# Kernel optimization log

Measured on AMD Instinct MI355X. Metric: run time of the kernel, lower is better.

Reference implementation:

```python
import jax, jax.numpy as jnp
import numpy as np

N = 100000        # nodes
E = 1600000       # edges (avg degree 16)
D_IN = 128        # input_dim
HID = 128         # hidden
L = 2             # num_layers
EPS = 1e-5        # LayerNorm eps (torch default)


def setup_inputs() -> dict:
    key = jax.random.key(0)
    ks = jax.random.split(key, 5)
    x = jax.random.normal(ks[0], (N, D_IN), dtype=jnp.float32)
    edge_index = jax.random.randint(ks[1], (2, E), 0, N, dtype=jnp.int64)
    e_feat = jax.random.uniform(ks[2], (E,), dtype=jnp.float32)
    # nn.Linear(input_dim, hidden): weight [hidden, input_dim], bias [hidden]
    lin_w = jax.random.normal(ks[3], (HID, D_IN), dtype=jnp.float32) / np.float32(np.sqrt(D_IN))
    lin_b = jax.random.normal(ks[4], (HID,), dtype=jnp.float32) * 0.01
    ln_scale = jnp.ones((L, HID), dtype=jnp.float32)
    ln_bias = jnp.zeros((L, HID), dtype=jnp.float32)
    return {"x": x, "edge_index": edge_index, "e_feat": e_feat,
            "lin_w": lin_w, "lin_b": lin_b,
            "ln_scale": ln_scale, "ln_bias": ln_bias}


def _layernorm(h, scale, bias):
    mu = jnp.mean(h, axis=-1, keepdims=True)
    var = jnp.mean(jnp.square(h - mu), axis=-1, keepdims=True)
    return (h - mu) * jax.lax.rsqrt(var + EPS) * scale + bias


def reference(x, edge_index, e_feat, lin_w, lin_b, ln_scale, ln_bias):
    src, dst = edge_index[0], edge_index[1]
    h = x @ lin_w.T + lin_b            # [N, HID]
    ori = h
    for i in range(L):
        if i != 0:                      # res=True
            h = h + ori
        h = _layernorm(h, ln_scale[i], ln_bias[i])   # norm=True
        h = jax.nn.relu(h)              # relu=True; dp=0 -> dropout no-op
        # GraphConv(weight=False, bias=False): weighted SpMM aggregation
        msg = h[src] * e_feat[:, None]  # [E, HID]
        h = jax.ops.segment_sum(msg, dst, num_segments=N)  # [N, HID]
    return h
```

## Files before the change

kernel.cpp:

```cpp
#include <hip/hip_runtime.h>


constexpr int N_NODES = 100000;
constexpr int N_EDGES = 1600000;
constexpr int HID     = 128;
constexpr int CAP     = 48;
constexpr float LN_EPS = 1e-5f;

typedef __attribute__((ext_vector_type(8))) short short8;
typedef __attribute__((ext_vector_type(4))) float floatx4;

__device__ inline unsigned pack_bf16x2(float a, float b) {
    unsigned ua = __float_as_uint(a), ub = __float_as_uint(b);
    ua += 0x7fff + ((ua >> 16) & 1);
    ub += 0x7fff + ((ub >> 16) & 1);
    return (ua >> 16) | (ub & 0xffff0000u);
}

__global__ void k_prepw(const float* __restrict__ W, unsigned* __restrict__ Wb) {
    int i = blockIdx.x * 256 + threadIdx.x;
    float2 w = ((const float2*)W)[i];
    Wb[i] = pack_bf16x2(w.x, w.y);
}

__global__ void k_scatter(const int* __restrict__ ei, const float* __restrict__ ef,
                          int* __restrict__ cnt, int2* __restrict__ cwp) {
    int e = blockIdx.x * 256 + threadIdx.x;
    if (e >= N_EDGES) return;
    int s = ei[e];
    int d = ei[N_EDGES + e];
    int pos = atomicAdd(&cnt[d], 1);
    if (pos < CAP) cwp[(size_t)d * CAP + pos] = make_int2(s, __float_as_int(ef[e]));
}

__global__ __launch_bounds__(256) void k_gemm_mfma(const float* __restrict__ x,
                                                   const unsigned* __restrict__ Wb,
                                                   const float* __restrict__ bias,
                                                   const float* __restrict__ lns,
                                                   const float* __restrict__ lnb,
                                                   float* __restrict__ h0,
                                                   unsigned* __restrict__ hact) {
    __shared__ __align__(16) char smem[128 * 136 * 2 + 64 * 136 * 2];
    ushort (*Ws)[136] = (ushort(*)[136])smem;
    ushort (*Xs)[136] = (ushort(*)[136])(smem + 128 * 136 * 2);
    float  (*Hs)[132] = (float(*)[132])smem;

    const int t    = threadIdx.x;
    const int row0 = blockIdx.x * 64;

    {
        const uint4* Wg = (const uint4*)Wb;
#pragma unroll
        for (int i = 0; i < 8; ++i) {
            int g = t + 256 * i;
            int r = g >> 4;
            int c = (g & 15) * 8;
            uint4 v = Wg[g];
            *(uint4*)&Ws[r][c] = v;
        }
    }
    {
        const float4* xg = (const float4*)x;
        const int base = blockIdx.x * 2048;
#pragma unroll
        for (int i = 0; i < 8; ++i) {
            int f = t + 256 * i;
            int g = base + f;
            float4 v = make_float4(0.f, 0.f, 0.f, 0.f);
            if (g < N_NODES * 32) v = xg[g];
            int r = f >> 5;
            int c = (f & 31) * 4;
            uint2 p = make_uint2(pack_bf16x2(v.x, v.y), pack_bf16x2(v.z, v.w));
            *(uint2*)&Xs[r][c] = p;
        }
    }
    __syncthreads();

    const int wv   = t >> 6;
    const int l    = t & 63;
    const int mrow = l & 15;
    const int kq   = l >> 4;

    floatx4 acc[8];
#pragma unroll
    for (int i = 0; i < 8; ++i) acc[i] = (floatx4){0.f, 0.f, 0.f, 0.f};

#pragma unroll
    for (int ks = 0; ks < 4; ++ks) {
        short8 a = *(const short8*)&Xs[wv * 16 + mrow][ks * 32 + kq * 8];
#pragma unroll
        for (int tc = 0; tc < 8; ++tc) {
            short8 b = *(const short8*)&Ws[tc * 16 + mrow][ks * 32 + kq * 8];
            acc[tc] = __builtin_amdgcn_mfma_f32_16x16x32_bf16(a, b, acc[tc], 0, 0, 0);
        }
    }
    __syncthreads();

#pragma unroll
    for (int tc = 0; tc < 8; ++tc)
#pragma unroll
        for (int r = 0; r < 4; ++r)
            Hs[wv * 16 + kq * 4 + r][tc * 16 + mrow] = acc[tc][r];
    __syncthreads();

    const float2 b2  = ((const float2*)bias)[l];
    const float2 sc2 = ((const float2*)lns)[l];
    const float2 bb2 = ((const float2*)lnb)[l];
    for (int rr = 0; rr < 16; ++rr) {
        const int lrow = wv * 16 + rr;
        const int grow = row0 + lrow;
        if (grow >= N_NODES) break;
        float2 v = *(const float2*)&Hs[lrow][l * 2];
        v.x += b2.x; v.y += b2.y;
        ((float2*)h0)[(size_t)grow * 64 + l] = v;
        float s  = v.x + v.y;
        float s2 = v.x * v.x + v.y * v.y;
#pragma unroll
        for (int m = 1; m < 64; m <<= 1) {
            s  += __shfl_xor(s, m);
            s2 += __shfl_xor(s2, m);
        }
        const float mu   = s * (1.0f / 128.0f);
        const float var  = s2 * (1.0f / 128.0f) - mu * mu;
        const float rstd = rsqrtf(var + LN_EPS);
        float y0 = fmaxf((v.x - mu) * rstd * sc2.x + bb2.x, 0.0f);
        float y1 = fmaxf((v.y - mu) * rstd * sc2.y + bb2.y, 0.0f);
        hact[(size_t)grow * 64 + l] = pack_bf16x2(y0, y1);
    }
}

__global__ __launch_bounds__(256) void k_spmm_ln(const int* __restrict__ cnt,
                                                 const int2* __restrict__ cwp,
                                                 const unsigned* __restrict__ Hb,
                                                 const float* __restrict__ ori,
                                                 const float* __restrict__ lns,
                                                 const float* __restrict__ lnb,
                                                 unsigned* __restrict__ hout) {
    const int wid  = (blockIdx.x * 256 + threadIdx.x) >> 6;
    const int lane = threadIdx.x & 63;

    const int deg = __builtin_amdgcn_readfirstlane(min(cnt[wid], CAP));
    const int beg = wid * CAP;
    const int end = beg + deg;

    float2 acc = make_float2(0.0f, 0.0f);
    int e = beg;
    for (; e + 4 <= end; e += 4) {
        int2 c0 = cwp[e], c1 = cwp[e + 1], c2 = cwp[e + 2], c3 = cwp[e + 3];
        unsigned v0 = Hb[(size_t)c0.x * 64 + lane];
        unsigned v1 = Hb[(size_t)c1.x * 64 + lane];
        unsigned v2 = Hb[(size_t)c2.x * 64 + lane];
        unsigned v3 = Hb[(size_t)c3.x * 64 + lane];
        float w0 = __int_as_float(c0.y), w1 = __int_as_float(c1.y);
        float w2 = __int_as_float(c2.y), w3 = __int_as_float(c3.y);
        acc.x += w0 * __uint_as_float(v0 << 16) + w1 * __uint_as_float(v1 << 16)
               + w2 * __uint_as_float(v2 << 16) + w3 * __uint_as_float(v3 << 16);
        acc.y += w0 * __uint_as_float(v0 & 0xffff0000u) + w1 * __uint_as_float(v1 & 0xffff0000u)
               + w2 * __uint_as_float(v2 & 0xffff0000u) + w3 * __uint_as_float(v3 & 0xffff0000u);
    }
    for (; e < end; ++e) {
        int2 c0 = cwp[e];
        unsigned v0 = Hb[(size_t)c0.x * 64 + lane];
        float w0 = __int_as_float(c0.y);
        acc.x += w0 * __uint_as_float(v0 << 16);
        acc.y += w0 * __uint_as_float(v0 & 0xffff0000u);
    }

    float2 o = ((const float2*)ori)[(size_t)wid * 64 + lane];
    float vx = acc.x + o.x, vy = acc.y + o.y;
    float s  = vx + vy;
    float s2 = vx * vx + vy * vy;
#pragma unroll
    for (int m = 1; m < 64; m <<= 1) {
        s  += __shfl_xor(s, m);
        s2 += __shfl_xor(s2, m);
    }
    const float mu   = s * (1.0f / 128.0f);
    const float var  = s2 * (1.0f / 128.0f) - mu * mu;
    const float rstd = rsqrtf(var + LN_EPS);
    const int c = lane * 2;
    float y0 = fmaxf((vx - mu) * rstd * lns[c]     + lnb[c],     0.0f);
    float y1 = fmaxf((vy - mu) * rstd * lns[c + 1] + lnb[c + 1], 0.0f);
    hout[(size_t)wid * 64 + lane] = pack_bf16x2(y0, y1);
}

__global__ __launch_bounds__(256) void k_spmm_out(const int* __restrict__ cnt,
                                                  const int2* __restrict__ cwp,
                                                  const unsigned* __restrict__ Hb,
                                                  float* __restrict__ out) {
    const int wid  = (blockIdx.x * 256 + threadIdx.x) >> 6;
    const int lane = threadIdx.x & 63;

    const int deg = __builtin_amdgcn_readfirstlane(min(cnt[wid], CAP));
    const int beg = wid * CAP;
    const int end = beg + deg;

    float2 acc = make_float2(0.0f, 0.0f);
    int e = beg;
    for (; e + 4 <= end; e += 4) {
        int2 c0 = cwp[e], c1 = cwp[e + 1], c2 = cwp[e + 2], c3 = cwp[e + 3];
        unsigned v0 = Hb[(size_t)c0.x * 64 + lane];
        unsigned v1 = Hb[(size_t)c1.x * 64 + lane];
        unsigned v2 = Hb[(size_t)c2.x * 64 + lane];
        unsigned v3 = Hb[(size_t)c3.x * 64 + lane];
        float w0 = __int_as_float(c0.y), w1 = __int_as_float(c1.y);
        float w2 = __int_as_float(c2.y), w3 = __int_as_float(c3.y);
        acc.x += w0 * __uint_as_float(v0 << 16) + w1 * __uint_as_float(v1 << 16)
               + w2 * __uint_as_float(v2 << 16) + w3 * __uint_as_float(v3 << 16);
        acc.y += w0 * __uint_as_float(v0 & 0xffff0000u) + w1 * __uint_as_float(v1 & 0xffff0000u)
               + w2 * __uint_as_float(v2 & 0xffff0000u) + w3 * __uint_as_float(v3 & 0xffff0000u);
    }
    for (; e < end; ++e) {
        int2 c0 = cwp[e];
        unsigned v0 = Hb[(size_t)c0.x * 64 + lane];
        float w0 = __int_as_float(c0.y);
        acc.x += w0 * __uint_as_float(v0 << 16);
        acc.y += w0 * __uint_as_float(v0 & 0xffff0000u);
    }
    ((float2*)out)[(size_t)wid * 64 + lane] = acc;
}

extern "C" void kernel_launch(void* const* d_in, const int* in_sizes, int n_in,
                              void* d_out, int out_size, void* d_ws, size_t ws_size,
                              hipStream_t stream) {
    const float* x   = (const float*)d_in[0];
    const int*   ei  = (const int*)d_in[1];
    const float* ef  = (const float*)d_in[2];
    const float* W   = (const float*)d_in[3];
    const float* b   = (const float*)d_in[4];
    const float* lns = (const float*)d_in[5];
    const float* lnb = (const float*)d_in[6];
    float* out = (float*)d_out;

    float* h0 = out;

    unsigned* hact  = (unsigned*)d_ws;
    unsigned* hact2 = hact + (size_t)N_NODES * 64;
    int*      cnt   = (int*)(hact2 + (size_t)N_NODES * 64);
    unsigned* Wb    = (unsigned*)(cnt + N_NODES);
    int2*     cwp   = (int2*)(Wb + 8192);

    const int eb = (N_EDGES + 255) / 256;
    const int wb = N_NODES * 64 / 256;

    hipMemsetAsync(cnt, 0, N_NODES * sizeof(int), stream);
    k_prepw<<<32, 256, 0, stream>>>(W, Wb);
    k_scatter<<<eb, 256, 0, stream>>>(ei, ef, cnt, cwp);

    k_gemm_mfma<<<(N_NODES + 63) / 64, 256, 0, stream>>>(x, Wb, b, lns, lnb, h0, hact);

    k_spmm_ln<<<wb, 256, 0, stream>>>(cnt, cwp, hact, h0, lns + HID, lnb + HID, hact2);
    k_spmm_out<<<wb, 256, 0, stream>>>(cnt, cwp, hact2, out);
}
```

Baseline: 388.2 us.

## Build compact CSR via two-level bucket sort instead of padded atomic scatter

```diff
diff --git a/kernel.cpp b/kernel.cpp
--- a/kernel.cpp
+++ b/kernel.cpp
@@ -4,7 +4,8 @@
 constexpr int N_NODES = 100000;
 constexpr int N_EDGES = 1600000;
 constexpr int HID     = 128;
-constexpr int CAP     = 48;
+constexpr int NBKT    = (N_NODES + 511) / 512;
+constexpr int BCAP    = 9216;
 constexpr float LN_EPS = 1e-5f;
 
 typedef __attribute__((ext_vector_type(8))) short short8;
@@ -23,14 +24,147 @@
     Wb[i] = pack_bf16x2(w.x, w.y);
 }
 
-__global__ void k_scatter(const int* __restrict__ ei, const float* __restrict__ ef,
-                          int* __restrict__ cnt, int2* __restrict__ cwp) {
-    int e = blockIdx.x * 256 + threadIdx.x;
-    if (e >= N_EDGES) return;
-    int s = ei[e];
-    int d = ei[N_EDGES + e];
-    int pos = atomicAdd(&cnt[d], 1);
-    if (pos < CAP) cwp[(size_t)d * CAP + pos] = make_int2(s, __float_as_int(ef[e]));
+__global__ __launch_bounds__(256) void k_bin(const int* __restrict__ ei,
+                                             const float* __restrict__ ef,
+                                             int* __restrict__ gcur,
+                                             int* __restrict__ gbufDst,
+                                             int2* __restrict__ gbufSW) {
+    __shared__ int cnt[NBKT];
+    __shared__ int incl[256];
+    __shared__ int gbase[NBKT];
+    __shared__ int sdst[2048];
+    __shared__ int2 ssw[2048];
+    const int t = threadIdx.x;
+
+    for (int e0 = blockIdx.x * 2048; e0 < N_EDGES; e0 += gridDim.x * 2048) {
+        for (int i = t; i < NBKT; i += 256) cnt[i] = 0;
+        __syncthreads();
+
+        const int nE = min(2048, N_EDGES - e0);
+        int ed[8], es[8], ep[8]; float ew[8];
+        const int base = e0 + t * 8;
+        if (base + 8 <= N_EDGES) {
+            int4 s0 = *(const int4*)&ei[base];
+            int4 s1 = *(const int4*)&ei[base + 4];
+            int4 d0 = *(const int4*)&ei[N_EDGES + base];
+            int4 d1 = *(const int4*)&ei[N_EDGES + base + 4];
+            float4 w0 = *(const float4*)&ef[base];
+            float4 w1 = *(const float4*)&ef[base + 4];
+            es[0]=s0.x; es[1]=s0.y; es[2]=s0.z; es[3]=s0.w;
+            es[4]=s1.x; es[5]=s1.y; es[6]=s1.z; es[7]=s1.w;
+            ed[0]=d0.x; ed[1]=d0.y; ed[2]=d0.z; ed[3]=d0.w;
+            ed[4]=d1.x; ed[5]=d1.y; ed[6]=d1.z; ed[7]=d1.w;
+            ew[0]=w0.x; ew[1]=w0.y; ew[2]=w0.z; ew[3]=w0.w;
+            ew[4]=w1.x; ew[5]=w1.y; ew[6]=w1.z; ew[7]=w1.w;
+#pragma unroll
+            for (int k = 0; k < 8; ++k) ep[k] = atomicAdd(&cnt[ed[k] >> 9], 1);
+        } else {
+#pragma unroll
+            for (int k = 0; k < 8; ++k) {
+                int idx = base + k;
+                if (idx < N_EDGES) {
+                    es[k] = ei[idx]; ed[k] = ei[N_EDGES + idx]; ew[k] = ef[idx];
+                    ep[k] = atomicAdd(&cnt[ed[k] >> 9], 1);
+                } else ed[k] = -1;
+            }
+        }
+        __syncthreads();
+
+        int v = (t < NBKT) ? cnt[t] : 0;
+        incl[t] = v;
+        for (int o = 1; o < 256; o <<= 1) {
+            __syncthreads();
+            int u = (t >= o) ? incl[t - o] : 0;
+            __syncthreads();
+            incl[t] += u;
+        }
+        __syncthreads();
+        if (t < NBKT) gbase[t] = atomicAdd(&gcur[t], v);
+        __syncthreads();
+
+#pragma unroll
+        for (int k = 0; k < 8; ++k) {
+            if (ed[k] < 0) continue;
+            int b = ed[k] >> 9;
+            int idx = incl[b] - cnt[b] + ep[k];
+            sdst[idx] = ed[k];
+            ssw[idx] = make_int2(es[k], __float_as_int(ew[k]));
+        }
+        __syncthreads();
+
+        for (int j = t; j < nE; j += 256) {
+            int d = sdst[j];
+            int b = d >> 9;
+            int pos = gbase[b] + (j - (incl[b] - cnt[b]));
+            if (pos < BCAP) {
+                gbufDst[(size_t)b * BCAP + pos] = d;
+                gbufSW [(size_t)b * BCAP + pos] = ssw[j];
+            }
+        }
+        __syncthreads();
+    }
+}
+
+__global__ __launch_bounds__(256) void k_scan(const int* __restrict__ gcur,
+                                              int* __restrict__ cbase,
+                                              int* __restrict__ rp) {
+    __shared__ int s[256];
+    const int t = threadIdx.x;
+    int v = (t < NBKT) ? min(gcur[t], BCAP) : 0;
+    s[t] = v;
+    for (int o = 1; o < 256; o <<= 1) {
+        __syncthreads();
+        int u = (t >= o) ? s[t - o] : 0;
+        __syncthreads();
+        s[t] += u;
+    }
+    __syncthreads();
+    if (t < NBKT) cbase[t] = s[t] - v;
+    if (t == NBKT - 1) rp[N_NODES] = s[t];
+}
+
+__global__ __launch_bounds__(512) void k_build(const int* __restrict__ gcur,
+                                               const int* __restrict__ cbase,
+                                               const int* __restrict__ gbufDst,
+                                               const int2* __restrict__ gbufSW,
+                                               int* __restrict__ rp,
+                                               int2* __restrict__ csr) {
+    __shared__ int cnt[512];
+    __shared__ int cur[512];
+    __shared__ int2 sorted[BCAP];
+    const int t     = threadIdx.x;
+    const int b     = blockIdx.x;
+    const int nbase = b * 512;
+    const int nb = min(gcur[b], BCAP);
+    const int cb = cbase[b];
+    const int*  bd = gbufDst + (size_t)b * BCAP;
+    const int2* bs = gbufSW  + (size_t)b * BCAP;
+
+    cnt[t] = 0;
+    __syncthreads();
+    for (int i = t; i < nb; i += 512) atomicAdd(&cnt[bd[i] - nbase], 1);
+    __syncthreads();
+
+    int v = cnt[t];
+    for (int o = 1; o < 512; o <<= 1) {
+        __syncthreads();
+        int u = (t >= o) ? cnt[t - o] : 0;
+        __syncthreads();
+        cnt[t] += u;
+    }
+    __syncthreads();
+    const int excl = cnt[t] - v;
+    cur[t] = excl;
+    if (nbase + t < N_NODES) rp[nbase + t] = cb + excl;
+    __syncthreads();
+
+    for (int i = t; i < nb; i += 512) {
+        int d = bd[i];
+        int pos = atomicAdd(&cur[d - nbase], 1);
+        sorted[pos] = bs[i];
+    }
+    __syncthreads();
+    for (int i = t; i < nb; i += 512) csr[(size_t)cb + i] = sorted[i];
 }
 
 __global__ __launch_bounds__(256) void k_gemm_mfma(const float* __restrict__ x,
@@ -55,8 +189,8 @@
             int g = t + 256 * i;
             int r = g >> 4;
             int c = (g & 15) * 8;
-            uint4 v = Wg[g];
-            *(uint4*)&Ws[r][c] = v;
+            uint4 vv = Wg[g];
+            *(uint4*)&Ws[r][c] = vv;
         }
     }
     {
@@ -66,11 +200,11 @@
         for (int i = 0; i < 8; ++i) {
             int f = t + 256 * i;
             int g = base + f;
-            float4 v = make_float4(0.f, 0.f, 0.f, 0.f);
-            if (g < N_NODES * 32) v = xg[g];
+            float4 vv = make_float4(0.f, 0.f, 0.f, 0.f);
+            if (g < N_NODES * 32) vv = xg[g];
             int r = f >> 5;
             int c = (f & 31) * 4;
-            uint2 p = make_uint2(pack_bf16x2(v.x, v.y), pack_bf16x2(v.z, v.w));
+            uint2 p = make_uint2(pack_bf16x2(vv.x, vv.y), pack_bf16x2(vv.z, vv.w));
             *(uint2*)&Xs[r][c] = p;
         }
     }
@@ -90,8 +224,8 @@
         short8 a = *(const short8*)&Xs[wv * 16 + mrow][ks * 32 + kq * 8];
 #pragma unroll
         for (int tc = 0; tc < 8; ++tc) {
-            short8 b = *(const short8*)&Ws[tc * 16 + mrow][ks * 32 + kq * 8];
-            acc[tc] = __builtin_amdgcn_mfma_f32_16x16x32_bf16(a, b, acc[tc], 0, 0, 0);
+            short8 bb = *(const short8*)&Ws[tc * 16 + mrow][ks * 32 + kq * 8];
+            acc[tc] = __builtin_amdgcn_mfma_f32_16x16x32_bf16(a, bb, acc[tc], 0, 0, 0);
         }
     }
     __syncthreads();
@@ -110,11 +244,11 @@
         const int lrow = wv * 16 + rr;
         const int grow = row0 + lrow;
         if (grow >= N_NODES) break;
-        float2 v = *(const float2*)&Hs[lrow][l * 2];
-        v.x += b2.x; v.y += b2.y;
-        ((float2*)h0)[(size_t)grow * 64 + l] = v;
-        float s  = v.x + v.y;
-        float s2 = v.x * v.x + v.y * v.y;
+        float2 vv = *(const float2*)&Hs[lrow][l * 2];
+        vv.x += b2.x; vv.y += b2.y;
+        ((float2*)h0)[(size_t)grow * 64 + l] = vv;
+        float s  = vv.x + vv.y;
+        float s2 = vv.x * vv.x + vv.y * vv.y;
 #pragma unroll
         for (int m = 1; m < 64; m <<= 1) {
             s  += __shfl_xor(s, m);
@@ -123,14 +257,14 @@
         const float mu   = s * (1.0f / 128.0f);
         const float var  = s2 * (1.0f / 128.0f) - mu * mu;
         const float rstd = rsqrtf(var + LN_EPS);
-        float y0 = fmaxf((v.x - mu) * rstd * sc2.x + bb2.x, 0.0f);
-        float y1 = fmaxf((v.y - mu) * rstd * sc2.y + bb2.y, 0.0f);
+        float y0 = fmaxf((vv.x - mu) * rstd * sc2.x + bb2.x, 0.0f);
+        float y1 = fmaxf((vv.y - mu) * rstd * sc2.y + bb2.y, 0.0f);
         hact[(size_t)grow * 64 + l] = pack_bf16x2(y0, y1);
     }
 }
 
-__global__ __launch_bounds__(256) void k_spmm_ln(const int* __restrict__ cnt,
-                                                 const int2* __restrict__ cwp,
+__global__ __launch_bounds__(256) void k_spmm_ln(const int* __restrict__ rp,
+                                                 const int2* __restrict__ cw,
                                                  const unsigned* __restrict__ Hb,
                                                  const float* __restrict__ ori,
                                                  const float* __restrict__ lns,
@@ -139,14 +273,13 @@
     const int wid  = (blockIdx.x * 256 + threadIdx.x) >> 6;
     const int lane = threadIdx.x & 63;
 
-    const int deg = __builtin_amdgcn_readfirstlane(min(cnt[wid], CAP));
-    const int beg = wid * CAP;
-    const int end = beg + deg;
+    const int beg = __builtin_amdgcn_readfirstlane(rp[wid]);
+    const int end = __builtin_amdgcn_readfirstlane(rp[wid + 1]);
 
     float2 acc = make_float2(0.0f, 0.0f);
     int e = beg;
     for (; e + 4 <= end; e += 4) {
-        int2 c0 = cwp[e], c1 = cwp[e + 1], c2 = cwp[e + 2], c3 = cwp[e + 3];
+        int2 c0 = cw[e], c1 = cw[e + 1], c2 = cw[e + 2], c3 = cw[e + 3];
         unsigned v0 = Hb[(size_t)c0.x * 64 + lane];
         unsigned v1 = Hb[(size_t)c1.x * 64 + lane];
         unsigned v2 = Hb[(size_t)c2.x * 64 + lane];
@@ -159,7 +292,7 @@
                + w2 * __uint_as_float(v2 & 0xffff0000u) + w3 * __uint_as_float(v3 & 0xffff0000u);
     }
     for (; e < end; ++e) {
-        int2 c0 = cwp[e];
+        int2 c0 = cw[e];
         unsigned v0 = Hb[(size_t)c0.x * 64 + lane];
         float w0 = __int_as_float(c0.y);
         acc.x += w0 * __uint_as_float(v0 << 16);
@@ -184,21 +317,20 @@
     hout[(size_t)wid * 64 + lane] = pack_bf16x2(y0, y1);
 }
 
-__global__ __launch_bounds__(256) void k_spmm_out(const int* __restrict__ cnt,
-                                                  const int2* __restrict__ cwp,
+__global__ __launch_bounds__(256) void k_spmm_out(const int* __restrict__ rp,
+                                                  const int2* __restrict__ cw,
                                                   const unsigned* __restrict__ Hb,
                                                   float* __restrict__ out) {
     const int wid  = (blockIdx.x * 256 + threadIdx.x) >> 6;
     const int lane = threadIdx.x & 63;
 
-    const int deg = __builtin_amdgcn_readfirstlane(min(cnt[wid], CAP));
-    const int beg = wid * CAP;
-    const int end = beg + deg;
+    const int beg = __builtin_amdgcn_readfirstlane(rp[wid]);
+    const int end = __builtin_amdgcn_readfirstlane(rp[wid + 1]);
 
     float2 acc = make_float2(0.0f, 0.0f);
     int e = beg;
     for (; e + 4 <= end; e += 4) {
-        int2 c0 = cwp[e], c1 = cwp[e + 1], c2 = cwp[e + 2], c3 = cwp[e + 3];
+        int2 c0 = cw[e], c1 = cw[e + 1], c2 = cw[e + 2], c3 = cw[e + 3];
         unsigned v0 = Hb[(size_t)c0.x * 64 + lane];
         unsigned v1 = Hb[(size_t)c1.x * 64 + lane];
         unsigned v2 = Hb[(size_t)c2.x * 64 + lane];
@@ -211,7 +343,7 @@
                + w2 * __uint_as_float(v2 & 0xffff0000u) + w3 * __uint_as_float(v3 & 0xffff0000u);
     }
     for (; e < end; ++e) {
-        int2 c0 = cwp[e];
+        int2 c0 = cw[e];
         unsigned v0 = Hb[(size_t)c0.x * 64 + lane];
         float w0 = __int_as_float(c0.y);
         acc.x += w0 * __uint_as_float(v0 << 16);
@@ -231,24 +363,28 @@
     const float* lns = (const float*)d_in[5];
     const float* lnb = (const float*)d_in[6];
     float* out = (float*)d_out;
-
-    float* h0 = out;
+    float* h0  = out;
 
     unsigned* hact  = (unsigned*)d_ws;
     unsigned* hact2 = hact + (size_t)N_NODES * 64;
-    int*      cnt   = (int*)(hact2 + (size_t)N_NODES * 64);
-    unsigned* Wb    = (unsigned*)(cnt + N_NODES);
-    int2*     cwp   = (int2*)(Wb + 8192);
-
-    const int eb = (N_EDGES + 255) / 256;
+    int2* csr    = (int2*)(hact2 + (size_t)N_NODES * 64);
+    int2* gbufSW = csr + N_EDGES;
+    unsigned* Wb = (unsigned*)(gbufSW + (size_t)NBKT * BCAP);
+    int* gcur    = (int*)(Wb + 8192);
+    int* cbase   = gcur + NBKT;
+    int* rp      = cbase + NBKT;
+    int* gbufDst = rp + (N_NODES + 1);
+
     const int wb = N_NODES * 64 / 256;
 
-    hipMemsetAsync(cnt, 0, N_NODES * sizeof(int), stream);
+    hipMemsetAsync(gcur, 0, NBKT * sizeof(int), stream);
     k_prepw<<<32, 256, 0, stream>>>(W, Wb);
-    k_scatter<<<eb, 256, 0, stream>>>(ei, ef, cnt, cwp);
+    k_bin<<<256, 256, 0, stream>>>(ei, ef, gcur, gbufDst, gbufSW);
+    k_scan<<<1, 256, 0, stream>>>(gcur, cbase, rp);
+    k_build<<<NBKT, 512, 0, stream>>>(gcur, cbase, gbufDst, gbufSW, rp, csr);
 
     k_gemm_mfma<<<(N_NODES + 63) / 64, 256, 0, stream>>>(x, Wb, b, lns, lnb, h0, hact);
 
-    k_spmm_ln<<<wb, 256, 0, stream>>>(cnt, cwp, hact, h0, lns + HID, lnb + HID, hact2);
-    k_spmm_out<<<wb, 256, 0, stream>>>(cnt, cwp, hact2, out);
-}
+    k_spmm_ln<<<wb, 256, 0, stream>>>(rp, csr, hact, h0, lns + HID, lnb + HID, hact2);
+    k_spmm_out<<<wb, 256, 0, stream>>>(rp, csr, hact2, out);
+}
```

Result: faster. 323.0 us (-16.8%).
